# Optimization experiments

Measured on AMD Instinct MI355X. Metric: run time of the kernel, lower is better.

The kernel has to match this reference:

```python
import jax, jax.numpy as jnp
import numpy as np

N_HEAD = 16

def setup_inputs() -> dict:
    key = jax.random.key(0)
    ks = jax.random.split(key, 5)
    C = 1024
    x = jax.random.normal(ks[0], (2, 2048, C), dtype=jnp.float32)
    w_attn = jax.random.normal(ks[1], (C, 3 * C), dtype=jnp.float32) * (C ** -0.5)
    b_attn = jax.random.normal(ks[2], (3 * C,), dtype=jnp.float32) * 0.02
    w_proj = jax.random.normal(ks[3], (C, C), dtype=jnp.float32) * (C ** -0.5)
    b_proj = jax.random.normal(ks[4], (C,), dtype=jnp.float32) * 0.02
    return {"x": x, "w_attn": w_attn, "b_attn": b_attn, "w_proj": w_proj, "b_proj": b_proj}

def reference(x, w_attn, b_attn, w_proj, b_proj):
    B, T, C = x.shape
    H = N_HEAD
    D = C // H  # head_dim
    qkv = x @ w_attn + b_attn  # [B,T,3C]
    q, k, v = jnp.split(qkv, 3, axis=-1)
    # [B,T,H,D] -> [B,H,T,D]
    q = q.reshape(B, T, H, D).transpose(0, 2, 1, 3)
    k = k.reshape(B, T, H, D).transpose(0, 2, 1, 3)
    v = v.reshape(B, T, H, D).transpose(0, 2, 1, 3)
    scale = 1.0 / np.sqrt(D).astype(np.float32)
    att = jnp.einsum('bhqd,bhkd->bhqk', q, k) * scale  # [B,H,T,T]
    causal = jnp.tril(jnp.ones((T, T), dtype=bool))
    att = jnp.where(causal, att, jnp.finfo(att.dtype).min)
    att = jax.nn.softmax(att, axis=-1)
    y = jnp.einsum('bhqk,bhkd->bhqd', att, v)  # [B,H,T,D]
    y = y.transpose(0, 2, 1, 3).reshape(B, T, C)
    return y @ w_proj + b_proj
```

## Files before the change

kernel.cpp:

```cpp
#include <hip/hip_runtime.h>
#include <hip/hip_bf16.h>
#include <stdint.h>

typedef __bf16 bf16x8 __attribute__((ext_vector_type(8)));
typedef __bf16 bf16x4 __attribute__((ext_vector_type(4)));
typedef float  f32x4  __attribute__((ext_vector_type(4)));

#define GLOBAL_AS __attribute__((address_space(1)))
#define LDS_AS    __attribute__((address_space(3)))

__device__ __forceinline__ void gld_lds16(const __bf16* g, __bf16* l) {
  __builtin_amdgcn_global_load_lds((GLOBAL_AS void*)g, (LDS_AS void*)l, 16, 0, 0);
}

#define QSCALE 0.18033688011116029f

__device__ __forceinline__ unsigned pk2(float a, float b) {
  unsigned short ua = __builtin_bit_cast(unsigned short, (__bf16)a);
  unsigned short ub = __builtin_bit_cast(unsigned short, (__bf16)b);
  return (unsigned)ua | ((unsigned)ub << 16);
}

union PackU { unsigned u[4]; bf16x8 v; };

__global__ __launch_bounds__(256) void cast_bf16_kernel(const float* __restrict__ src,
                                                        __bf16* __restrict__ dst, int n)
{
  int i = (blockIdx.x * 256 + threadIdx.x) * 8;
  if (i >= n) return;
  float4 a = *(const float4*)(src + i);
  float4 b = *(const float4*)(src + i + 4);
  bf16x8 o;
  o[0]=(__bf16)a.x; o[1]=(__bf16)a.y; o[2]=(__bf16)a.z; o[3]=(__bf16)a.w;
  o[4]=(__bf16)b.x; o[5]=(__bf16)b.y; o[6]=(__bf16)b.z; o[7]=(__bf16)b.w;
  *(bf16x8*)(dst + i) = o;
}

__global__ __launch_bounds__(256) void transpose_cast_kernel(const float* __restrict__ src,
                                                             __bf16* __restrict__ dst,
                                                             int R, int C)
{
  __shared__ float tile[32][33];
  int c0 = blockIdx.x * 32, r0 = blockIdx.y * 32;
  int tx = threadIdx.x & 31, ty = threadIdx.x >> 5;
  #pragma unroll
  for (int i = 0; i < 32; i += 8)
    tile[ty + i][tx] = src[(size_t)(r0 + ty + i) * C + (c0 + tx)];
  __syncthreads();
  #pragma unroll
  for (int i = 0; i < 32; i += 8)
    dst[(size_t)(c0 + ty + i) * R + (r0 + tx)] = (__bf16)tile[tx][ty + i];
}

template<int MODE, int BM>
__global__ __launch_bounds__(256, (BM == 128 ? 3 : 2))
void gemm_kernel(const __bf16* __restrict__ A,
                 const __bf16* __restrict__ Bt,
                 const float*  __restrict__ bias,
                 float* __restrict__ outF,
                 __bf16* __restrict__ qb,
                 __bf16* __restrict__ kb,
                 __bf16* __restrict__ vb,
                 int M, int N, int K)
{
  __shared__ __bf16 As[BM * 64];
  __shared__ __bf16 Bs[128 * 64];
  const int tid  = threadIdx.x;
  const int wave = tid >> 6, lane = tid & 63;
  const int lo = lane & 15, g4 = lane >> 4;
  int bm, bn;
  if (MODE == 0) {
    int bid = blockIdx.x;
    int bm_i = (bid & 7) * 4 + ((bid >> 3) & 3);
    int bn_i = bid >> 5;
    bm = bm_i * 128; bn = bn_i * 128;
  } else {
    bm = blockIdx.y * BM; bn = blockIdx.x * 128;
  }
  const int wr = (wave >> 1) * (BM / 2);
  const int wc = (wave & 1) * 64;
  constexpr int MF = BM / 32;

  f32x4 acc[MF][4] = {};

  const int nkt = K >> 6;
  for (int kt = 0; kt < nkt; ++kt) {
    const int k0 = kt << 6;
    __syncthreads();
    #pragma unroll
    for (int j = 0; j < BM / 32; ++j) {
      int c = j * 256 + tid;
      int r = c >> 3, cc = c & 7;
      int cs = cc ^ (r & 7);
      gld_lds16(A + (size_t)(bm + r) * K + (k0 + cs * 8), As + c * 8);
    }
    #pragma unroll
    for (int j = 0; j < 4; ++j) {
      int c = j * 256 + tid;
      int r = c >> 3, cc = c & 7;
      int cs = cc ^ (r & 7);
      gld_lds16(Bt + (size_t)(bn + r) * K + (k0 + cs * 8), Bs + c * 8);
    }
    __syncthreads();
    #pragma unroll
    for (int ks = 0; ks < 2; ++ks) {
      bf16x8 af[MF], bfr[4];
      #pragma unroll
      for (int mf = 0; mf < MF; ++mf) {
        int row = wr + mf * 16 + lo;
        int ch = (ks * 4 + g4) ^ (row & 7);
        af[mf] = *(const bf16x8*)(As + row * 64 + ch * 8);
      }
      #pragma unroll
      for (int nf = 0; nf < 4; ++nf) {
        int row = wc + nf * 16 + lo;
        int ch = (ks * 4 + g4) ^ (row & 7);
        bfr[nf] = *(const bf16x8*)(Bs + row * 64 + ch * 8);
      }
      #pragma unroll
      for (int mf = 0; mf < MF; ++mf)
        #pragma unroll
        for (int nf = 0; nf < 4; ++nf)
          acc[mf][nf] = __builtin_amdgcn_mfma_f32_16x16x32_bf16(af[mf], bfr[nf], acc[mf][nf], 0, 0, 0);
    }
  }

  float bv[4];
  #pragma unroll
  for (int nf = 0; nf < 4; ++nf) bv[nf] = bias[bn + wc + nf * 16 + lo];

  if (MODE == 1) {
    #pragma unroll
    for (int mf = 0; mf < MF; ++mf)
      #pragma unroll
      for (int nf = 0; nf < 4; ++nf) {
        int col = bn + wc + nf * 16 + lo;
        #pragma unroll
        for (int j = 0; j < 4; ++j) {
          int row = bm + wr + mf * 16 + g4 * 4 + j;
          outF[(size_t)row * N + col] = acc[mf][nf][j] + bv[nf];
        }
      }
  } else {
    #pragma unroll
    for (int mf = 0; mf < MF; ++mf) {
      const int tbase = bm + wr + mf * 16 + g4 * 4;
      const int b = tbase >> 11, t = tbase & 2047;
      #pragma unroll
      for (int nf = 0; nf < 4; ++nf) {
        int n = bn + wc + nf * 16 + lo;
        int sel = n >> 10, hd = n & 1023;
        int h = hd >> 6, d = hd & 63;
        size_t bh = (size_t)(b * 16 + h);
        if (sel == 2) {
          bf16x4 pv;
          #pragma unroll
          for (int j = 0; j < 4; ++j) pv[j] = (__bf16)(acc[mf][nf][j] + bv[nf]);
          *(bf16x4*)(vb + (bh * 64 + d) * 2048 + t) = pv;
        } else if (sel == 0) {
          #pragma unroll
          for (int j = 0; j < 4; ++j)
            qb[(bh * 2048 + (size_t)(t + j)) * 64 + d] = (__bf16)((acc[mf][nf][j] + bv[nf]) * QSCALE);
        } else {
          #pragma unroll
          for (int j = 0; j < 4; ++j)
            kb[(bh * 2048 + (size_t)(t + j)) * 64 + d] = (__bf16)(acc[mf][nf][j] + bv[nf]);
        }
      }
    }
  }
}

__global__ __launch_bounds__(256, 4)
void attn_kernel(const __bf16* __restrict__ qg_, const __bf16* __restrict__ kg,
                 const __bf16* __restrict__ vg, __bf16* __restrict__ yg,
                 __bf16* __restrict__ pY, float* __restrict__ pL)
{
  const int n = blockIdx.x;
  const int xcd = n & 7;
  const int m = n >> 3;
  const int bh = xcd + 8 * (m & 3);
  const int t = m >> 2;
  const int b = bh >> 4, h = bh & 15;

  const int tid  = threadIdx.x;
  const int wave = tid >> 6;
  const int lane = tid & 63;
  const int l15  = lane & 15;
  const int g    = lane >> 4;
  const int sw   = l15 & 7;

  __shared__ __bf16 Kb[2][64 * 64];
  __shared__ __bf16 Vb[2][64 * 64];

  const __bf16* qbase = qg_ + (size_t)bh * 2048 * 64;
  const __bf16* kbase = kg  + (size_t)bh * 2048 * 64;
  const __bf16* vbase = vg  + (size_t)bh * 64 * 2048;

  bf16x8 qf0, qf1;
  f32x4 o0, o1, o2, o3, osum;

  bf16x8 ones;
  #pragma unroll
  for (int j = 0; j < 8; ++j) ones[j] = (__bf16)1.0f;

  auto LOADQ = [&](int strip) {
    const int q16 = strip * 64 + wave * 16 + l15;
    qf0 = *(const bf16x8*)(qbase + (size_t)q16 * 64 + g * 8);
    qf1 = *(const bf16x8*)(qbase + (size_t)q16 * 64 + 32 + g * 8);
  };
  auto RESET = [&]() {
    o0 = f32x4{}; o1 = f32x4{}; o2 = f32x4{}; o3 = f32x4{}; osum = f32x4{};
  };
  auto STAGE = [&](int kt, int bsel) {
    #pragma unroll
    for (int j = 0; j < 2; ++j) {
      int c = j * 256 + tid;
      int cr = c >> 3, cc = c & 7;
      int cs = cc ^ (cr & 7);
      int pr = (cr & 0x23) | ((cr & 0x10) >> 2) | ((cr & 0x0C) << 1);
      gld_lds16(kbase + (size_t)(kt * 64 + pr) * 64 + cs * 8, &Kb[bsel][0] + c * 8);
      gld_lds16(vbase + (size_t)cr * 2048 + (kt * 64 + cs * 8), &Vb[bsel][0] + c * 8);
    }
  };

  auto TILE = [&](int cur, bool diag) {
    const __bf16* KL = &Kb[cur][0];
    f32x4 s0 = {}, s1 = {}, s2 = {}, s3 = {};
    {
      bf16x8 k00 = *(const bf16x8*)(KL + (0  + l15) * 64 + ((0 + g) ^ sw) * 8);
      bf16x8 k01 = *(const bf16x8*)(KL + (0  + l15) * 64 + ((4 + g) ^ sw) * 8);
      bf16x8 k10 = *(const bf16x8*)(KL + (16 + l15) * 64 + ((0 + g) ^ sw) * 8);
      bf16x8 k11 = *(const bf16x8*)(KL + (16 + l15) * 64 + ((4 + g) ^ sw) * 8);
      bf16x8 k20 = *(const bf16x8*)(KL + (32 + l15) * 64 + ((0 + g) ^ sw) * 8);
      bf16x8 k21 = *(const bf16x8*)(KL + (32 + l15) * 64 + ((4 + g) ^ sw) * 8);
      bf16x8 k30 = *(const bf16x8*)(KL + (48 + l15) * 64 + ((0 + g) ^ sw) * 8);
      bf16x8 k31 = *(const bf16x8*)(KL + (48 + l15) * 64 + ((4 + g) ^ sw) * 8);
      __builtin_amdgcn_s_setprio(1);
      s0 = __builtin_amdgcn_mfma_f32_16x16x32_bf16(k00, qf0, s0, 0, 0, 0);
      s0 = __builtin_amdgcn_mfma_f32_16x16x32_bf16(k01, qf1, s0, 0, 0, 0);
      s1 = __builtin_amdgcn_mfma_f32_16x16x32_bf16(k10, qf0, s1, 0, 0, 0);
      s1 = __builtin_amdgcn_mfma_f32_16x16x32_bf16(k11, qf1, s1, 0, 0, 0);
      s2 = __builtin_amdgcn_mfma_f32_16x16x32_bf16(k20, qf0, s2, 0, 0, 0);
      s2 = __builtin_amdgcn_mfma_f32_16x16x32_bf16(k21, qf1, s2, 0, 0, 0);
      s3 = __builtin_amdgcn_mfma_f32_16x16x32_bf16(k30, qf0, s3, 0, 0, 0);
      s3 = __builtin_amdgcn_mfma_f32_16x16x32_bf16(k31, qf1, s3, 0, 0, 0);
      __builtin_amdgcn_s_setprio(0);
    }

    if (diag) {
      const int qr = wave * 16 + l15;
      #pragma unroll
      for (int r2 = 0; r2 < 4; ++r2) {
        if (8 * g + r2          > qr) s0[r2] = -3.0e38f;
        if (8 * g + 4 + r2      > qr) s1[r2] = -3.0e38f;
        if (32 + 8 * g + r2     > qr) s2[r2] = -3.0e38f;
        if (32 + 8 * g + 4 + r2 > qr) s3[r2] = -3.0e38f;
      }
    }

    #pragma unroll
    for (int r2 = 0; r2 < 4; ++r2) s0[r2] = exp2f(s0[r2]);
    #pragma unroll
    for (int r2 = 0; r2 < 4; ++r2) s1[r2] = exp2f(s1[r2]);
    #pragma unroll
    for (int r2 = 0; r2 < 4; ++r2) s2[r2] = exp2f(s2[r2]);
    #pragma unroll
    for (int r2 = 0; r2 < 4; ++r2) s3[r2] = exp2f(s3[r2]);

    PackU pa0, pa1;
    pa0.u[0] = pk2(s0[0], s0[1]); pa0.u[1] = pk2(s0[2], s0[3]);
    pa0.u[2] = pk2(s1[0], s1[1]); pa0.u[3] = pk2(s1[2], s1[3]);
    pa1.u[0] = pk2(s2[0], s2[1]); pa1.u[1] = pk2(s2[2], s2[3]);
    pa1.u[2] = pk2(s3[0], s3[1]); pa1.u[3] = pk2(s3[2], s3[3]);

    const __bf16* VL = &Vb[cur][0];
    bf16x8 v00 = *(const bf16x8*)(VL + (0  + l15) * 64 + ((0 + g) ^ sw) * 8);
    bf16x8 v01 = *(const bf16x8*)(VL + (0  + l15) * 64 + ((4 + g) ^ sw) * 8);
    bf16x8 v10 = *(const bf16x8*)(VL + (16 + l15) * 64 + ((0 + g) ^ sw) * 8);
    bf16x8 v11 = *(const bf16x8*)(VL + (16 + l15) * 64 + ((4 + g) ^ sw) * 8);
    bf16x8 v20 = *(const bf16x8*)(VL + (32 + l15) * 64 + ((0 + g) ^ sw) * 8);
    bf16x8 v21 = *(const bf16x8*)(VL + (32 + l15) * 64 + ((4 + g) ^ sw) * 8);
    bf16x8 v30 = *(const bf16x8*)(VL + (48 + l15) * 64 + ((0 + g) ^ sw) * 8);
    bf16x8 v31 = *(const bf16x8*)(VL + (48 + l15) * 64 + ((4 + g) ^ sw) * 8);

    __builtin_amdgcn_s_setprio(1);
    osum = __builtin_amdgcn_mfma_f32_16x16x32_bf16(pa0.v, ones, osum, 0, 0, 0);
    osum = __builtin_amdgcn_mfma_f32_16x16x32_bf16(pa1.v, ones, osum, 0, 0, 0);
    o0 = __builtin_amdgcn_mfma_f32_16x16x32_bf16(pa0.v, v00, o0, 0, 0, 0);
    o0 = __builtin_amdgcn_mfma_f32_16x16x32_bf16(pa1.v, v01, o0, 0, 0, 0);
    o1 = __builtin_amdgcn_mfma_f32_16x16x32_bf16(pa0.v, v10, o1, 0, 0, 0);
    o1 = __builtin_amdgcn_mfma_f32_16x16x32_bf16(pa1.v, v11, o1, 0, 0, 0);
    o2 = __builtin_amdgcn_mfma_f32_16x16x32_bf16(pa0.v, v20, o2, 0, 0, 0);
    o2 = __builtin_amdgcn_mfma_f32_16x16x32_bf16(pa1.v, v21, o2, 0, 0, 0);
    o3 = __builtin_amdgcn_mfma_f32_16x16x32_bf16(pa0.v, v30, o3, 0, 0, 0);
    o3 = __builtin_amdgcn_mfma_f32_16x16x32_bf16(pa1.v, v31, o3, 0, 0, 0);
    __builtin_amdgcn_s_setprio(0);
  };

  auto WRITE_Y = [&](int strip) {
    #pragma unroll
    for (int r2 = 0; r2 < 4; ++r2) {
      float il = 1.0f / osum[r2];
      int trow = strip * 64 + wave * 16 + 4 * g + r2;
      __bf16* dst = yg + ((size_t)(b * 2048 + trow)) * 1024 + h * 64;
      dst[l15]      = (__bf16)(o0[r2] * il);
      dst[16 + l15] = (__bf16)(o1[r2] * il);
      dst[32 + l15] = (__bf16)(o2[r2] * il);
      dst[48 + l15] = (__bf16)(o3[r2] * il);
    }
  };
  auto WRITE_PART = [&](int slot) {
    __bf16* po = pY + (size_t)slot * 4096;
    #pragma unroll
    for (int r2 = 0; r2 < 4; ++r2) {
      int row = wave * 16 + 4 * g + r2;
      __bf16* dst = po + row * 64;
      dst[l15]      = (__bf16)o0[r2];
      dst[16 + l15] = (__bf16)o1[r2];
      dst[32 + l15] = (__bf16)o2[r2];
      dst[48 + l15] = (__bf16)o3[r2];
    }
    if (l15 == 0) {
      #pragma unroll
      for (int r2 = 0; r2 < 4; ++r2)
        pL[slot * 64 + wave * 16 + 4 * g + r2] = osum[r2];
    }
  };

  int cur = 0;
  if (t < 16) {
    LOADQ(t); RESET();
    bf16x8 qB0, qB1;
    {
      const int q16b = (31 - t) * 64 + wave * 16 + l15;
      qB0 = *(const bf16x8*)(qbase + (size_t)q16b * 64 + g * 8);
      qB1 = *(const bf16x8*)(qbase + (size_t)q16b * 64 + 32 + g * 8);
    }
    STAGE(0, 0);
    for (int j = 0; j < 17; ++j) {
      __syncthreads();
      if (j < 16) {
        int nx = j + 1;
        STAGE((nx <= t) ? nx : (nx + 15 - t), cur ^ 1);
      }
      if (j <= t) {
        TILE(cur, j == t);
        if (j == t) { WRITE_Y(t); qf0 = qB0; qf1 = qB1; RESET(); }
      } else {
        TILE(cur, j == 16);
      }
      cur ^= 1;
    }
    WRITE_PART((bh * 16 + (15 - t)) * 2 + 1);
  } else {
    LOADQ(t); RESET();
    STAGE(0, 0);
    for (int j = 0; j < 16; ++j) {
      __syncthreads();
      if (j < 15) STAGE(j + 1, cur ^ 1);
      TILE(cur, false);
      cur ^= 1;
    }
    WRITE_PART((bh * 16 + (t - 16)) * 2);
  }
}

__global__ __launch_bounds__(256)
void attn_merge_kernel(const __bf16* __restrict__ pY, const float* __restrict__ pL,
                       __bf16* __restrict__ yg)
{
  const int us = blockIdx.x & 15, bh = blockIdx.x >> 4;
  const int b = bh >> 4, h = bh & 15;
  const int tid = threadIdx.x;
  const int row = tid >> 2, d0 = (tid & 3) * 16;
  const int slotA = (bh * 16 + us) * 2, slotB = slotA + 1;

  float l = pL[slotA * 64 + row] + pL[slotB * 64 + row];
  float inv = 1.0f / l;

  const __bf16* pa = pY + (size_t)slotA * 4096 + row * 64 + d0;
  const __bf16* pb = pY + (size_t)slotB * 4096 + row * 64 + d0;
  __bf16* dst = yg + ((size_t)(b * 2048 + (16 + us) * 64 + row)) * 1024 + h * 64 + d0;

  bf16x8 a0 = *(const bf16x8*)pa, a1 = *(const bf16x8*)(pa + 8);
  bf16x8 b0 = *(const bf16x8*)pb, b1 = *(const bf16x8*)(pb + 8);
  bf16x8 r0, r1;
  #pragma unroll
  for (int j = 0; j < 8; ++j) {
    r0[j] = (__bf16)(((float)a0[j] + (float)b0[j]) * inv);
    r1[j] = (__bf16)(((float)a1[j] + (float)b1[j]) * inv);
  }
  *(bf16x8*)dst = r0;
  *(bf16x8*)(dst + 8) = r1;
}

extern "C" void kernel_launch(void* const* d_in, const int* in_sizes, int n_in,
                              void* d_out, int out_size, void* d_ws, size_t ws_size,
                              hipStream_t stream)
{
  const float* x      = (const float*)d_in[0];
  const float* w_attn = (const float*)d_in[1];
  const float* b_attn = (const float*)d_in[2];
  const float* w_proj = (const float*)d_in[3];
  const float* b_proj = (const float*)d_in[4];
  float* out = (float*)d_out;

  __bf16* xb  = (__bf16*)d_ws;
  __bf16* waT = xb  + (size_t)4096 * 1024;
  __bf16* wpT = waT + (size_t)3072 * 1024;
  __bf16* qb  = wpT + (size_t)1024 * 1024;
  __bf16* kb  = qb  + (size_t)32 * 2048 * 64;
  __bf16* vb  = kb  + (size_t)32 * 2048 * 64;
  __bf16* yb  = vb  + (size_t)32 * 2048 * 64;

  __bf16* pY = xb;
  float*  pL = (float*)waT;

  cast_bf16_kernel<<<2048, 256, 0, stream>>>(x, xb, 4096 * 1024);
  transpose_cast_kernel<<<dim3(96, 32), 256, 0, stream>>>(w_attn, waT, 1024, 3072);
  transpose_cast_kernel<<<dim3(32, 32), 256, 0, stream>>>(w_proj, wpT, 1024, 1024);
  gemm_kernel<0, 128><<<768, 256, 0, stream>>>(xb, waT, b_attn, nullptr,
                                               qb, kb, vb, 4096, 3072, 1024);
  attn_kernel<<<1024, 256, 0, stream>>>(qb, kb, vb, yb, pY, pL);
  attn_merge_kernel<<<512, 256, 0, stream>>>(pY, pL, yb);
  gemm_kernel<1, 64><<<dim3(8, 64), 256, 0, stream>>>(yb, wpT, b_proj, out,
                                                      nullptr, nullptr, nullptr, 4096, 1024, 1024);
}
```

Before: 99.88 us.

## Fuse attention split merge into projection GEMM and merge prep kernels

Folds the three cast/transpose prep launches into one prep kernel that picks its role by block index. Removes the separate attention-merge kernel: for rows of the second half of the sequence, the projection GEMM now combines the two partial attention outputs and their normalisers while loading A tiles into LDS. This drops two launches and one round trip of the merged activations through memory. In exchange those GEMM blocks use synchronous register loads with extra arithmetic instead of async global-to-LDS loads, which may slow their main loop.

```diff
diff --git a/kernel.cpp b/kernel.cpp
--- a/kernel.cpp
+++ b/kernel.cpp
@@ -23,26 +23,35 @@
 
 union PackU { unsigned u[4]; bf16x8 v; };
 
-__global__ __launch_bounds__(256) void cast_bf16_kernel(const float* __restrict__ src,
-                                                        __bf16* __restrict__ dst, int n)
+__global__ __launch_bounds__(256)
+void prep_kernel(const float* __restrict__ x, __bf16* __restrict__ xb,
+                 const float* __restrict__ wa, __bf16* __restrict__ waT,
+                 const float* __restrict__ wp, __bf16* __restrict__ wpT)
 {
-  int i = (blockIdx.x * 256 + threadIdx.x) * 8;
-  if (i >= n) return;
-  float4 a = *(const float4*)(src + i);
-  float4 b = *(const float4*)(src + i + 4);
-  bf16x8 o;
-  o[0]=(__bf16)a.x; o[1]=(__bf16)a.y; o[2]=(__bf16)a.z; o[3]=(__bf16)a.w;
-  o[4]=(__bf16)b.x; o[5]=(__bf16)b.y; o[6]=(__bf16)b.z; o[7]=(__bf16)b.w;
-  *(bf16x8*)(dst + i) = o;
-}
-
-__global__ __launch_bounds__(256) void transpose_cast_kernel(const float* __restrict__ src,
-                                                             __bf16* __restrict__ dst,
-                                                             int R, int C)
-{
+  const int id = blockIdx.x;
+  const int tid = threadIdx.x;
+  if (id < 2048) {
+    int i = (id * 256 + tid) * 8;
+    float4 a = *(const float4*)(x + i);
+    float4 b = *(const float4*)(x + i + 4);
+    bf16x8 o;
+    o[0]=(__bf16)a.x; o[1]=(__bf16)a.y; o[2]=(__bf16)a.z; o[3]=(__bf16)a.w;
+    o[4]=(__bf16)b.x; o[5]=(__bf16)b.y; o[6]=(__bf16)b.z; o[7]=(__bf16)b.w;
+    *(bf16x8*)(xb + i) = o;
+    return;
+  }
   __shared__ float tile[32][33];
-  int c0 = blockIdx.x * 32, r0 = blockIdx.y * 32;
-  int tx = threadIdx.x & 31, ty = threadIdx.x >> 5;
+  const float* src; __bf16* dst; int R, C, c0, r0;
+  if (id < 5120) {
+    int idx = id - 2048;
+    src = wa; dst = waT; R = 1024; C = 3072;
+    c0 = (idx % 96) * 32; r0 = (idx / 96) * 32;
+  } else {
+    int idx = id - 5120;
+    src = wp; dst = wpT; R = 1024; C = 1024;
+    c0 = (idx & 31) * 32; r0 = (idx >> 5) * 32;
+  }
+  int tx = tid & 31, ty = tid >> 5;
   #pragma unroll
   for (int i = 0; i < 32; i += 8)
     tile[ty + i][tx] = src[(size_t)(r0 + ty + i) * C + (c0 + tx)];
@@ -61,6 +70,8 @@
                  __bf16* __restrict__ qb,
                  __bf16* __restrict__ kb,
                  __bf16* __restrict__ vb,
+                 const __bf16* __restrict__ pYp,
+                 const float* __restrict__ pLp,
                  int M, int N, int K)
 {
   __shared__ __bf16 As[BM * 64];
@@ -80,6 +91,7 @@
   const int wr = (wave >> 1) * (BM / 2);
   const int wc = (wave & 1) * 64;
   constexpr int MF = BM / 32;
+  const bool mergedBlk = (MODE == 2) && ((bm >> 10) & 1);
 
   f32x4 acc[MF][4] = {};
 
@@ -87,12 +99,35 @@
   for (int kt = 0; kt < nkt; ++kt) {
     const int k0 = kt << 6;
     __syncthreads();
-    #pragma unroll
-    for (int j = 0; j < BM / 32; ++j) {
-      int c = j * 256 + tid;
-      int r = c >> 3, cc = c & 7;
-      int cs = cc ^ (r & 7);
-      gld_lds16(A + (size_t)(bm + r) * K + (k0 + cs * 8), As + c * 8);
+    if (mergedBlk) {
+      #pragma unroll
+      for (int j = 0; j < BM / 32; ++j) {
+        int c = j * 256 + tid;
+        int r = c >> 3, cc = c & 7;
+        int cs = cc ^ (r & 7);
+        int gy = bm + r;
+        int b = gy >> 11, row64 = gy & 63;
+        int us = ((gy & 2047) >> 6) - 16;
+        int slotA = ((b * 16 + kt) * 16 + us) * 2;
+        const __bf16* pa = pYp + (size_t)slotA * 4096 + row64 * 64 + cs * 8;
+        const __bf16* pb = pa + 4096;
+        float inv = 1.0f / (pLp[slotA * 64 + row64] + pLp[(slotA + 1) * 64 + row64]);
+        bf16x8 av = *(const bf16x8*)pa;
+        bf16x8 bv2 = *(const bf16x8*)pb;
+        bf16x8 mv;
+        #pragma unroll
+        for (int jj = 0; jj < 8; ++jj)
+          mv[jj] = (__bf16)(((float)av[jj] + (float)bv2[jj]) * inv);
+        *(bf16x8*)(As + c * 8) = mv;
+      }
+    } else {
+      #pragma unroll
+      for (int j = 0; j < BM / 32; ++j) {
+        int c = j * 256 + tid;
+        int r = c >> 3, cc = c & 7;
+        int cs = cc ^ (r & 7);
+        gld_lds16(A + (size_t)(bm + r) * K + (k0 + cs * 8), As + c * 8);
+      }
     }
     #pragma unroll
     for (int j = 0; j < 4; ++j) {
@@ -129,7 +164,7 @@
   #pragma unroll
   for (int nf = 0; nf < 4; ++nf) bv[nf] = bias[bn + wc + nf * 16 + lo];
 
-  if (MODE == 1) {
+  if (MODE == 2) {
     #pragma unroll
     for (int mf = 0; mf < MF; ++mf)
       #pragma unroll
@@ -366,35 +401,6 @@
   }
 }
 
-__global__ __launch_bounds__(256)
-void attn_merge_kernel(const __bf16* __restrict__ pY, const float* __restrict__ pL,
-                       __bf16* __restrict__ yg)
-{
-  const int us = blockIdx.x & 15, bh = blockIdx.x >> 4;
-  const int b = bh >> 4, h = bh & 15;
-  const int tid = threadIdx.x;
-  const int row = tid >> 2, d0 = (tid & 3) * 16;
-  const int slotA = (bh * 16 + us) * 2, slotB = slotA + 1;
-
-  float l = pL[slotA * 64 + row] + pL[slotB * 64 + row];
-  float inv = 1.0f / l;
-
-  const __bf16* pa = pY + (size_t)slotA * 4096 + row * 64 + d0;
-  const __bf16* pb = pY + (size_t)slotB * 4096 + row * 64 + d0;
-  __bf16* dst = yg + ((size_t)(b * 2048 + (16 + us) * 64 + row)) * 1024 + h * 64 + d0;
-
-  bf16x8 a0 = *(const bf16x8*)pa, a1 = *(const bf16x8*)(pa + 8);
-  bf16x8 b0 = *(const bf16x8*)pb, b1 = *(const bf16x8*)(pb + 8);
-  bf16x8 r0, r1;
-  #pragma unroll
-  for (int j = 0; j < 8; ++j) {
-    r0[j] = (__bf16)(((float)a0[j] + (float)b0[j]) * inv);
-    r1[j] = (__bf16)(((float)a1[j] + (float)b1[j]) * inv);
-  }
-  *(bf16x8*)dst = r0;
-  *(bf16x8*)(dst + 8) = r1;
-}
-
 extern "C" void kernel_launch(void* const* d_in, const int* in_sizes, int n_in,
                               void* d_out, int out_size, void* d_ws, size_t ws_size,
                               hipStream_t stream)
@@ -417,13 +423,12 @@
   __bf16* pY = xb;
   float*  pL = (float*)waT;
 
-  cast_bf16_kernel<<<2048, 256, 0, stream>>>(x, xb, 4096 * 1024);
-  transpose_cast_kernel<<<dim3(96, 32), 256, 0, stream>>>(w_attn, waT, 1024, 3072);
-  transpose_cast_kernel<<<dim3(32, 32), 256, 0, stream>>>(w_proj, wpT, 1024, 1024);
+  prep_kernel<<<6144, 256, 0, stream>>>(x, xb, w_attn, waT, w_proj, wpT);
   gemm_kernel<0, 128><<<768, 256, 0, stream>>>(xb, waT, b_attn, nullptr,
-                                               qb, kb, vb, 4096, 3072, 1024);
+                                               qb, kb, vb, nullptr, nullptr,
+                                               4096, 3072, 1024);
   attn_kernel<<<1024, 256, 0, stream>>>(qb, kb, vb, yb, pY, pL);
-  attn_merge_kernel<<<512, 256, 0, stream>>>(pY, pL, yb);
-  gemm_kernel<1, 64><<<dim3(8, 64), 256, 0, stream>>>(yb, wpT, b_proj, out,
-                                                      nullptr, nullptr, nullptr, 4096, 1024, 1024);
-}
+  gemm_kernel<2, 64><<<dim3(8, 64), 256, 0, stream>>>(yb, wpT, b_proj, out,
+                                                      nullptr, nullptr, nullptr, pY, pL,
+                                                      4096, 1024, 1024);
+}
```

Measured after the change: 101.8 us. About the same (+1.9%).
